# Kernel optimization log

Hardware: AMD Instinct MI355X
Metric: run time of the kernel (lower is better)

Reference implementation:

```python
import jax, jax.numpy as jnp
import numpy as np
from jax import lax

DT = 0.01  # fixed Euler-Maruyama step size

B, N, C, M, H, T = 1024, 64, 16, 16, 512, 128


def setup_inputs() -> dict:
    key = jax.random.key(0)
    ks = jax.random.split(key, 8)
    d_in = N + C  # concat(y, control)
    inp = {
        "y0": jax.random.normal(ks[0], (B, N), jnp.float32),
        "controls": jax.random.normal(ks[1], (T, C), jnp.float32),
        "noise": jax.random.normal(ks[2], (T - 1, B, M), jnp.float32),
        # mu MLP: d_in -> H -> N
        "W1_mu": jax.random.normal(ks[3], (d_in, H), jnp.float32) / np.sqrt(d_in),
        "b1_mu": jnp.zeros((H,), jnp.float32),
        "W2_mu": jax.random.normal(ks[4], (H, N), jnp.float32) / np.sqrt(H),
        "b2_mu": jnp.zeros((N,), jnp.float32),
        # sigma MLP: d_in -> H -> N*M
        "W1_sg": jax.random.normal(ks[5], (d_in, H), jnp.float32) / np.sqrt(d_in),
        "b1_sg": jnp.zeros((H,), jnp.float32),
        "W2_sg": jax.random.normal(ks[6], (H, N * M), jnp.float32) / np.sqrt(H),
        "b2_sg": jnp.zeros((N * M,), jnp.float32),
    }
    return inp


def _mlp(x, W1, b1, W2, b2):
    return jnp.maximum(x @ W1 + b1, 0.0) @ W2 + b2


def reference(y0, controls, noise, W1_mu, b1_mu, W2_mu, b2_mu,
              W1_sg, b1_sg, W2_sg, b2_sg):
    """Euler-Maruyama solve of dy = f(y,u) dt + g(y,u) dW.
    Returns trajectory [T, B, N] including y0 (as torchsde.sdeint does)."""
    b, n = y0.shape
    m = noise.shape[-1]
    sqrt_dt = jnp.sqrt(jnp.asarray(DT, y0.dtype))

    def step(y, inp):
        u, z = inp  # u: [C] control at t_k, z: [B, M] standard normal
        x = jnp.concatenate([y, jnp.broadcast_to(u[None, :], (b, u.shape[0]))], axis=1)
        drift = _mlp(x, W1_mu, b1_mu, W2_mu, b2_mu)              # [B, N]
        diff = _mlp(x, W1_sg, b1_sg, W2_sg, b2_sg).reshape(b, n, m)  # [B, N, M]
        dW = z * sqrt_dt
        y_next = y + drift * DT + jnp.einsum('bnm,bm->bn', diff, dW)
        return y_next, y_next

    _, ys = lax.scan(step, y0, (controls[:-1], noise))
    return jnp.concatenate([y0[None], ys], axis=0)  # [T, B, N]
```

## Files before the change

### kernel.cpp

```cpp
#include <hip/hip_runtime.h>


typedef _Float16 f16x8 __attribute__((ext_vector_type(8)));
typedef float    f32x4 __attribute__((ext_vector_type(4)));

#define MFMA(a,b,c) __builtin_amdgcn_mfma_f32_16x16x32_f16(a,b,c,0,0,0)

#define Bb 1024
#define Tt 128
#define NG 64
#define GB 8
#define Rr 16
#define NT 512

#define W2SG_OFF 0
#define W2SG_HALVES (64*16*2*512)
#define W2MU_OFF (W2SG_OFF + W2SG_HALVES)
#define W2MU_HALVES (4*16*2*512)
#define W1MU_OFF (W2MU_OFF + W2MU_HALVES)
#define W1_HALVES (32*3*2*512)
#define W1SG_OFF (W1MU_OFF + W1_HALVES)
#define WS_HALVES (W1SG_OFF + W1_HALVES)
#define ACC_BYTES_OFF ((size_t)WS_HALVES * 2)
#define ACC_FLOATS (3 * NG * 1024)
#define CNT_BYTES_OFF (ACC_BYTES_OFF + (size_t)ACC_FLOATS * 4)
#define CNT_STRIDE 16

__global__ __launch_bounds__(256) void pack_weights(
    const float* __restrict__ W1_mu, const float* __restrict__ W2_mu,
    const float* __restrict__ W1_sg, const float* __restrict__ W2_sg,
    _Float16* __restrict__ wsh)
{
    int gid = blockIdx.x * 256 + threadIdx.x;
    if (gid >= 81920) return;
    const float* src; int ncols, kvalid; size_t dst;
    int id, tile, ks, lane;
    if (gid < 65536) {
        id = gid; tile = id >> 10; id &= 1023; ks = id >> 6; lane = id & 63;
        src = W2_sg; ncols = 1024; kvalid = 512;
        dst = W2SG_OFF + (size_t)((tile*16 + ks)*2) * 512 + lane*8;
    } else if (gid < 69632) {
        id = gid - 65536; tile = id >> 10; id &= 1023; ks = id >> 6; lane = id & 63;
        src = W2_mu; ncols = 64; kvalid = 512;
        dst = W2MU_OFF + (size_t)((tile*16 + ks)*2) * 512 + lane*8;
    } else if (gid < 75776) {
        id = gid - 69632; tile = id / 192; id %= 192; ks = id >> 6; lane = id & 63;
        src = W1_mu; ncols = 512; kvalid = 80;
        dst = W1MU_OFF + (size_t)((tile*3 + ks)*2) * 512 + lane*8;
    } else {
        id = gid - 75776; tile = id / 192; id %= 192; ks = id >> 6; lane = id & 63;
        src = W1_sg; ncols = 512; kvalid = 80;
        dst = W1SG_OFF + (size_t)((tile*3 + ks)*2) * 512 + lane*8;
    }
    const int n  = tile*16 + (lane & 15);
    const int kb = ks*32 + ((lane >> 4) << 3);
    f16x8 hi8, lo8;
    #pragma unroll
    for (int jj = 0; jj < 8; ++jj) {
        int k = kb + jj;
        float wv = (k < kvalid) ? src[(size_t)k * ncols + n] : 0.f;
        _Float16 h = (_Float16)wv;
        hi8[jj] = h;
        lo8[jj] = (_Float16)(wv - (float)h);
    }
    *((f16x8*)(wsh + dst))       = hi8;
    *((f16x8*)(wsh + dst + 512)) = lo8;
}

__global__ __launch_bounds__(NT, 4) void nsde_splitk(
    const float* __restrict__ y0, const float* __restrict__ controls,
    const float* __restrict__ noise,
    const float* __restrict__ b1_mu, const float* __restrict__ b2_mu,
    const float* __restrict__ b1_sg, const float* __restrict__ b2_sg,
    const _Float16* __restrict__ wf,
    float* __restrict__ accbuf, unsigned int* __restrict__ cnt,
    float* __restrict__ out)
{
    __shared__ _Float16 s_xhi[Rr][104], s_xlo[Rr][104];
    __shared__ _Float16 s_hhi[2][Rr][72], s_hlo[2][Rr][72];
    __shared__ float s_y[Rr*64];
    __shared__ float s_dw[Rr][16];
    __shared__ float s_part[Rr*64];
    __shared__ float s_pmu[Rr*64];

    const int tid  = threadIdx.x;
    const int lane = tid & 63, w = tid >> 6;
    const int m15  = lane & 15, quad = lane >> 4;
    const int j    = blockIdx.x & 7;
    const int g    = blockIdx.x >> 3;
    const int r0   = g * Rr;

    const int l  = w >> 2;
    const int ct = w & 3;
    const int tg = j*4 + ct;
    const _Float16* w1base = wf + (l ? W1SG_OFF : W1MU_OFF);
    const float bias1 = (l ? b1_sg : b1_mu)[j*64 + ct*16 + m15];
    float b2v[8];
    #pragma unroll
    for (int t = 0; t < 8; ++t)
        b2v[t] = (j == 0) ? b2_sg[(w + t*8)*16 + m15] : 0.f;
    const float b2m = (w < 4 && j == 0) ? b2_mu[w*16 + m15] * 0.01f : 0.f;

    for (int e = tid; e < Rr*24; e += NT) {
        int r = e / 24, c = 80 + e % 24;
        s_xhi[r][c] = (_Float16)0.f; s_xlo[r][c] = (_Float16)0.f;
    }
    if (tid < 256) {
        int e0 = tid*4, r = e0 >> 6, n = e0 & 63;
        float4 yv = *(const float4*)&y0[(size_t)(r0 + r)*64 + n];
        float vv[4] = {yv.x, yv.y, yv.z, yv.w};
        #pragma unroll
        for (int q = 0; q < 4; ++q) {
            s_y[e0+q] = vv[q];
            _Float16 h = (_Float16)vv[q];
            s_xhi[r][n+q] = h; s_xlo[r][n+q] = (_Float16)(vv[q] - (float)h);
        }
        if ((tid >> 5) == j)
            *(float4*)&out[(size_t)(r0 + r)*64 + n] = yv;
        int rr2 = tid >> 4, cc2 = tid & 15;
        float u = controls[cc2];
        _Float16 h = (_Float16)u;
        s_xhi[rr2][64+cc2] = h; s_xlo[rr2][64+cc2] = (_Float16)(u - (float)h);
        s_dw[rr2][cc2] = noise[(size_t)(r0 + rr2)*16 + cc2] * 0.1f;
    }
    __syncthreads();

    for (int k = 0; k < Tt-1; ++k) {
        {
            f32x4 a0 = {0,0,0,0}, a1 = {0,0,0,0}, a2 = {0,0,0,0};
            #pragma unroll
            for (int ks = 0; ks < 3; ++ks) {
                const _Float16* bp = w1base + (size_t)((tg*3 + ks)*2)*512 + lane*8;
                f16x8 bh = *(const f16x8*)bp;
                f16x8 bl = *(const f16x8*)(bp + 512);
                f16x8 ah = *(const f16x8*)&s_xhi[m15][ks*32 + quad*8];
                f16x8 al = *(const f16x8*)&s_xlo[m15][ks*32 + quad*8];
                a0 = MFMA(ah, bh, a0);
                a1 = MFMA(ah, bl, a1);
                a2 = MFMA(al, bh, a2);
            }
            f32x4 s = a0 + a1 + a2;
            #pragma unroll
            for (int rg = 0; rg < 4; ++rg) {
                int row = quad*4 + rg;
                float v = fmaxf(s[rg] + bias1, 0.f);
                _Float16 h = (_Float16)v;
                s_hhi[l][row][ct*16 + m15] = h;
                s_hlo[l][row][ct*16 + m15] = (_Float16)(v - (float)h);
            }
        }
        __syncthreads();

        float dwv[4];
        #pragma unroll
        for (int rg = 0; rg < 4; ++rg)
            dwv[rg] = s_dw[quad*4 + rg][m15];

        if (w < 4) {
            f16x8 Mh0 = *(const f16x8*)&s_hhi[0][m15][quad*8];
            f16x8 Ml0 = *(const f16x8*)&s_hlo[0][m15][quad*8];
            f16x8 Mh1 = *(const f16x8*)&s_hhi[0][m15][32 + quad*8];
            f16x8 Ml1 = *(const f16x8*)&s_hlo[0][m15][32 + quad*8];
            const _Float16* bp = wf + W2MU_OFF + (size_t)((w*16 + 2*j)*2)*512 + lane*8;
            f16x8 bh0 = *(const f16x8*)(bp);
            f16x8 bl0 = *(const f16x8*)(bp + 512);
            f16x8 bh1 = *(const f16x8*)(bp + 1024);
            f16x8 bl1 = *(const f16x8*)(bp + 1536);
            f32x4 hh = {0,0,0,0}, hl = {0,0,0,0}, lh = {0,0,0,0};
            hh = MFMA(Mh0, bh0, hh); hl = MFMA(Mh0, bl0, hl); lh = MFMA(Ml0, bh0, lh);
            hh = MFMA(Mh1, bh1, hh); hl = MFMA(Mh1, bl1, hl); lh = MFMA(Ml1, bh1, lh);
            f32x4 s = hh + hl + lh;
            #pragma unroll
            for (int rg = 0; rg < 4; ++rg)
                s_pmu[(quad*4 + rg)*64 + w*16 + m15] = s[rg]*0.01f + b2m;
        }

        f16x8 Ah0 = *(const f16x8*)&s_hhi[1][m15][quad*8];
        f16x8 Al0 = *(const f16x8*)&s_hlo[1][m15][quad*8];
        f16x8 Ah1 = *(const f16x8*)&s_hhi[1][m15][32 + quad*8];
        f16x8 Al1 = *(const f16x8*)&s_hlo[1][m15][32 + quad*8];
        #pragma unroll 2
        for (int t = 0; t < 8; ++t) {
            const int nt = w + t*8;
            const _Float16* bp = wf + W2SG_OFF + (size_t)((nt*16 + 2*j)*2)*512 + lane*8;
            f16x8 bh0 = *(const f16x8*)(bp);
            f16x8 bl0 = *(const f16x8*)(bp + 512);
            f16x8 bh1 = *(const f16x8*)(bp + 1024);
            f16x8 bl1 = *(const f16x8*)(bp + 1536);
            f32x4 hh = {0,0,0,0}, hl = {0,0,0,0}, lh = {0,0,0,0};
            hh = MFMA(Ah0, bh0, hh); hl = MFMA(Ah0, bl0, hl); lh = MFMA(Al0, bh0, lh);
            hh = MFMA(Ah1, bh1, hh); hl = MFMA(Ah1, bl1, hl); lh = MFMA(Al1, bh1, lh);
            f32x4 s = hh + hl + lh;
            #pragma unroll
            for (int rg = 0; rg < 4; ++rg) {
                float v = (s[rg] + b2v[t]) * dwv[rg];
                v += __shfl_xor(v, 1); v += __shfl_xor(v, 2);
                v += __shfl_xor(v, 4); v += __shfl_xor(v, 8);
                if (m15 == 0) s_part[(quad*4 + rg)*64 + nt] = v;
            }
        }
        __syncthreads();

        const int slot = k % 3;
        float* ab = accbuf + ((size_t)slot*NG + g)*1024;
        const int e0 = tid*2;
        {
            float v0 = s_part[e0]   + s_pmu[e0];
            float v1 = s_part[e0+1] + s_pmu[e0+1];
            __hip_atomic_fetch_add(&ab[e0],   v0, __ATOMIC_RELAXED,
                                   __HIP_MEMORY_SCOPE_AGENT);
            __hip_atomic_fetch_add(&ab[e0+1], v1, __ATOMIC_RELAXED,
                                   __HIP_MEMORY_SCOPE_AGENT);
        }
        __syncthreads();
        if (tid == 0) {
            __hip_atomic_fetch_add(&cnt[g*CNT_STRIDE], 1u, __ATOMIC_RELEASE,
                                   __HIP_MEMORY_SCOPE_AGENT);
            while (__hip_atomic_load(&cnt[g*CNT_STRIDE], __ATOMIC_RELAXED,
                                     __HIP_MEMORY_SCOPE_AGENT) < (unsigned)GB*(k+1))
                __builtin_amdgcn_s_sleep(2);
        }
        __syncthreads();

        {
            const int r = e0 >> 6, n = e0 & 63;
            float sum0 = __hip_atomic_load(&ab[e0], __ATOMIC_RELAXED,
                                           __HIP_MEMORY_SCOPE_AGENT);
            float sum1 = __hip_atomic_load(&ab[e0+1], __ATOMIC_RELAXED,
                                           __HIP_MEMORY_SCOPE_AGENT);
            float ya = s_y[e0]   + sum0;
            float yb = s_y[e0+1] + sum1;
            s_y[e0] = ya; s_y[e0+1] = yb;
            _Float16 ha = (_Float16)ya, hb = (_Float16)yb;
            s_xhi[r][n] = ha;   s_xlo[r][n]   = (_Float16)(ya - (float)ha);
            s_xhi[r][n+1] = hb; s_xlo[r][n+1] = (_Float16)(yb - (float)hb);
            if ((tid >> 6) == j) {
                float2 o = {ya, yb};
                *(float2*)&out[((size_t)(k+1)*Bb + r0 + r)*64 + n] = o;
                if (k >= 1) {
                    float* zb = accbuf + ((size_t)((k-1)%3)*NG + g)*1024;
                    __hip_atomic_store(&zb[e0],   0.f, __ATOMIC_RELAXED,
                                       __HIP_MEMORY_SCOPE_AGENT);
                    __hip_atomic_store(&zb[e0+1], 0.f, __ATOMIC_RELAXED,
                                       __HIP_MEMORY_SCOPE_AGENT);
                }
            }
        }
        if (k < Tt-2 && tid < 256) {
            int r = tid >> 4, c = tid & 15;
            float u = controls[(size_t)(k+1)*16 + c];
            _Float16 h = (_Float16)u;
            s_xhi[r][64+c] = h; s_xlo[r][64+c] = (_Float16)(u - (float)h);
            s_dw[r][c] = noise[((size_t)(k+1)*Bb + r0 + r)*16 + c] * 0.1f;
        }
        __syncthreads();
    }
}

extern "C" void kernel_launch(void* const* d_in, const int* in_sizes, int n_in,
                              void* d_out, int out_size, void* d_ws, size_t ws_size,
                              hipStream_t stream) {
    const float* y0       = (const float*)d_in[0];
    const float* controls = (const float*)d_in[1];
    const float* noise    = (const float*)d_in[2];
    const float* W1_mu    = (const float*)d_in[3];
    const float* b1_mu    = (const float*)d_in[4];
    const float* W2_mu    = (const float*)d_in[5];
    const float* b2_mu    = (const float*)d_in[6];
    const float* W1_sg    = (const float*)d_in[7];
    const float* b1_sg    = (const float*)d_in[8];
    const float* W2_sg    = (const float*)d_in[9];
    const float* b2_sg    = (const float*)d_in[10];
    float* out = (float*)d_out;
    _Float16* wsh = (_Float16*)d_ws;
    float* accbuf = (float*)((char*)d_ws + ACC_BYTES_OFF);
    unsigned int* cnt = (unsigned int*)((char*)d_ws + CNT_BYTES_OFF);

    hipMemsetAsync((char*)d_ws + ACC_BYTES_OFF, 0,
                   (size_t)ACC_FLOATS*4 + (size_t)NG*CNT_STRIDE*4, stream);
    pack_weights<<<320, 256, 0, stream>>>(W1_mu, W2_mu, W1_sg, W2_sg, wsh);
    nsde_splitk<<<NG*GB, NT, 0, stream>>>(y0, controls, noise,
                                          b1_mu, b2_mu, b1_sg, b2_sg,
                                          (const _Float16*)wsh,
                                          accbuf, cnt, out);
}
```

Before: 2.297 ms.

## Keep weight fragments resident in registers and double rows per block

The per-step weight fragments (W1, W2_mu, W2_sg hi/lo) are loaded once into registers before the time loop instead of being reloaded from global memory every step. Each block now handles 32 rows instead of 16, so there are half as many blocks (256) and each runs two M-tiles per step. Next-step control and noise loads are issued before the barrier to overlap with compute. In exchange, register pressure rises sharply (launch bounds drop to 2 blocks per CU) and there are fewer groups, and therefore fewer blocks, spinning on the cross-block counter.

```diff
diff --git a/kernel.cpp b/kernel.cpp
--- a/kernel.cpp
+++ b/kernel.cpp
@@ -8,9 +8,9 @@
 
 #define Bb 1024
 #define Tt 128
-#define NG 64
+#define NG 32
 #define GB 8
-#define Rr 16
+#define Rr 32
 #define NT 512
 
 #define W2SG_OFF 0
@@ -22,7 +22,7 @@
 #define W1SG_OFF (W1MU_OFF + W1_HALVES)
 #define WS_HALVES (W1SG_OFF + W1_HALVES)
 #define ACC_BYTES_OFF ((size_t)WS_HALVES * 2)
-#define ACC_FLOATS (3 * NG * 1024)
+#define ACC_FLOATS (3 * NG * Rr * 64)
 #define CNT_BYTES_OFF (ACC_BYTES_OFF + (size_t)ACC_FLOATS * 4)
 #define CNT_STRIDE 16
 
@@ -67,7 +67,7 @@
     *((f16x8*)(wsh + dst + 512)) = lo8;
 }
 
-__global__ __launch_bounds__(NT, 4) void nsde_splitk(
+__global__ __launch_bounds__(NT, 2) void nsde_regw(
     const float* __restrict__ y0, const float* __restrict__ controls,
     const float* __restrict__ noise,
     const float* __restrict__ b1_mu, const float* __restrict__ b2_mu,
@@ -93,7 +93,6 @@
     const int l  = w >> 2;
     const int ct = w & 3;
     const int tg = j*4 + ct;
-    const _Float16* w1base = wf + (l ? W1SG_OFF : W1MU_OFF);
     const float bias1 = (l ? b1_sg : b1_mu)[j*64 + ct*16 + m15];
     float b2v[8];
     #pragma unroll
@@ -101,12 +100,43 @@
         b2v[t] = (j == 0) ? b2_sg[(w + t*8)*16 + m15] : 0.f;
     const float b2m = (w < 4 && j == 0) ? b2_mu[w*16 + m15] * 0.01f : 0.f;
 
+    f16x8 w1h[3], w1l[3];
+    {
+        const _Float16* w1base = wf + (l ? W1SG_OFF : W1MU_OFF);
+        #pragma unroll
+        for (int ks = 0; ks < 3; ++ks) {
+            const _Float16* bp = w1base + (size_t)((tg*3 + ks)*2)*512 + lane*8;
+            w1h[ks] = *(const f16x8*)bp;
+            w1l[ks] = *(const f16x8*)(bp + 512);
+        }
+    }
+    f16x8 wsg[8][4];
+    #pragma unroll
+    for (int t = 0; t < 8; ++t) {
+        const _Float16* bp = wf + W2SG_OFF
+            + (size_t)(((w + t*8)*16 + 2*j)*2)*512 + lane*8;
+        wsg[t][0] = *(const f16x8*)(bp);
+        wsg[t][1] = *(const f16x8*)(bp + 512);
+        wsg[t][2] = *(const f16x8*)(bp + 1024);
+        wsg[t][3] = *(const f16x8*)(bp + 1536);
+    }
+    f16x8 wmu[4];
+    {
+        const int wm = w & 3;
+        const _Float16* bp = wf + W2MU_OFF
+            + (size_t)((wm*16 + 2*j)*2)*512 + lane*8;
+        wmu[0] = *(const f16x8*)(bp);
+        wmu[1] = *(const f16x8*)(bp + 512);
+        wmu[2] = *(const f16x8*)(bp + 1024);
+        wmu[3] = *(const f16x8*)(bp + 1536);
+    }
+
     for (int e = tid; e < Rr*24; e += NT) {
         int r = e / 24, c = 80 + e % 24;
         s_xhi[r][c] = (_Float16)0.f; s_xlo[r][c] = (_Float16)0.f;
     }
-    if (tid < 256) {
-        int e0 = tid*4, r = e0 >> 6, n = e0 & 63;
+    {
+        const int e0 = tid*4, r = e0 >> 6, n = e0 & 63;
         float4 yv = *(const float4*)&y0[(size_t)(r0 + r)*64 + n];
         float vv[4] = {yv.x, yv.y, yv.z, yv.w};
         #pragma unroll
@@ -115,101 +145,101 @@
             _Float16 h = (_Float16)vv[q];
             s_xhi[r][n+q] = h; s_xlo[r][n+q] = (_Float16)(vv[q] - (float)h);
         }
-        if ((tid >> 5) == j)
+        if ((tid >> 6) == j)
             *(float4*)&out[(size_t)(r0 + r)*64 + n] = yv;
-        int rr2 = tid >> 4, cc2 = tid & 15;
-        float u = controls[cc2];
+        const int r2 = tid >> 4, c2 = tid & 15;
+        float u = controls[c2];
         _Float16 h = (_Float16)u;
-        s_xhi[rr2][64+cc2] = h; s_xlo[rr2][64+cc2] = (_Float16)(u - (float)h);
-        s_dw[rr2][cc2] = noise[(size_t)(r0 + rr2)*16 + cc2] * 0.1f;
+        s_xhi[r2][64+c2] = h; s_xlo[r2][64+c2] = (_Float16)(u - (float)h);
+        s_dw[r2][c2] = noise[(size_t)(r0 + r2)*16 + c2] * 0.1f;
     }
     __syncthreads();
 
     for (int k = 0; k < Tt-1; ++k) {
-        {
+        #pragma unroll
+        for (int mt = 0; mt < 2; ++mt) {
             f32x4 a0 = {0,0,0,0}, a1 = {0,0,0,0}, a2 = {0,0,0,0};
             #pragma unroll
             for (int ks = 0; ks < 3; ++ks) {
-                const _Float16* bp = w1base + (size_t)((tg*3 + ks)*2)*512 + lane*8;
-                f16x8 bh = *(const f16x8*)bp;
-                f16x8 bl = *(const f16x8*)(bp + 512);
-                f16x8 ah = *(const f16x8*)&s_xhi[m15][ks*32 + quad*8];
-                f16x8 al = *(const f16x8*)&s_xlo[m15][ks*32 + quad*8];
-                a0 = MFMA(ah, bh, a0);
-                a1 = MFMA(ah, bl, a1);
-                a2 = MFMA(al, bh, a2);
+                f16x8 ah = *(const f16x8*)&s_xhi[mt*16 + m15][ks*32 + quad*8];
+                f16x8 al = *(const f16x8*)&s_xlo[mt*16 + m15][ks*32 + quad*8];
+                a0 = MFMA(ah, w1h[ks], a0);
+                a1 = MFMA(ah, w1l[ks], a1);
+                a2 = MFMA(al, w1h[ks], a2);
             }
             f32x4 s = a0 + a1 + a2;
             #pragma unroll
             for (int rg = 0; rg < 4; ++rg) {
-                int row = quad*4 + rg;
+                int row = mt*16 + quad*4 + rg;
                 float v = fmaxf(s[rg] + bias1, 0.f);
                 _Float16 h = (_Float16)v;
                 s_hhi[l][row][ct*16 + m15] = h;
                 s_hlo[l][row][ct*16 + m15] = (_Float16)(v - (float)h);
             }
         }
-        __syncthreads();
-
-        float dwv[4];
-        #pragma unroll
-        for (int rg = 0; rg < 4; ++rg)
-            dwv[rg] = s_dw[quad*4 + rg][m15];
-
-        if (w < 4) {
-            f16x8 Mh0 = *(const f16x8*)&s_hhi[0][m15][quad*8];
-            f16x8 Ml0 = *(const f16x8*)&s_hlo[0][m15][quad*8];
-            f16x8 Mh1 = *(const f16x8*)&s_hhi[0][m15][32 + quad*8];
-            f16x8 Ml1 = *(const f16x8*)&s_hlo[0][m15][32 + quad*8];
-            const _Float16* bp = wf + W2MU_OFF + (size_t)((w*16 + 2*j)*2)*512 + lane*8;
-            f16x8 bh0 = *(const f16x8*)(bp);
-            f16x8 bl0 = *(const f16x8*)(bp + 512);
-            f16x8 bh1 = *(const f16x8*)(bp + 1024);
-            f16x8 bl1 = *(const f16x8*)(bp + 1536);
-            f32x4 hh = {0,0,0,0}, hl = {0,0,0,0}, lh = {0,0,0,0};
-            hh = MFMA(Mh0, bh0, hh); hl = MFMA(Mh0, bl0, hl); lh = MFMA(Ml0, bh0, lh);
-            hh = MFMA(Mh1, bh1, hh); hl = MFMA(Mh1, bl1, hl); lh = MFMA(Ml1, bh1, lh);
-            f32x4 s = hh + hl + lh;
+        float u_nx = 0.f, dw_nx = 0.f;
+        const int r2 = tid >> 4, c2 = tid & 15;
+        if (k < Tt-2) {
+            u_nx  = controls[(size_t)(k+1)*16 + c2];
+            dw_nx = noise[((size_t)(k+1)*Bb + r0 + r2)*16 + c2] * 0.1f;
+        }
+        __syncthreads();
+
+        #pragma unroll
+        for (int mt = 0; mt < 2; ++mt) {
+            const int rb = mt*16;
+            float dwv[4];
             #pragma unroll
             for (int rg = 0; rg < 4; ++rg)
-                s_pmu[(quad*4 + rg)*64 + w*16 + m15] = s[rg]*0.01f + b2m;
-        }
-
-        f16x8 Ah0 = *(const f16x8*)&s_hhi[1][m15][quad*8];
-        f16x8 Al0 = *(const f16x8*)&s_hlo[1][m15][quad*8];
-        f16x8 Ah1 = *(const f16x8*)&s_hhi[1][m15][32 + quad*8];
-        f16x8 Al1 = *(const f16x8*)&s_hlo[1][m15][32 + quad*8];
-        #pragma unroll 2
-        for (int t = 0; t < 8; ++t) {
-            const int nt = w + t*8;
-            const _Float16* bp = wf + W2SG_OFF + (size_t)((nt*16 + 2*j)*2)*512 + lane*8;
-            f16x8 bh0 = *(const f16x8*)(bp);
-            f16x8 bl0 = *(const f16x8*)(bp + 512);
-            f16x8 bh1 = *(const f16x8*)(bp + 1024);
-            f16x8 bl1 = *(const f16x8*)(bp + 1536);
-            f32x4 hh = {0,0,0,0}, hl = {0,0,0,0}, lh = {0,0,0,0};
-            hh = MFMA(Ah0, bh0, hh); hl = MFMA(Ah0, bl0, hl); lh = MFMA(Al0, bh0, lh);
-            hh = MFMA(Ah1, bh1, hh); hl = MFMA(Ah1, bl1, hl); lh = MFMA(Al1, bh1, lh);
-            f32x4 s = hh + hl + lh;
-            #pragma unroll
-            for (int rg = 0; rg < 4; ++rg) {
-                float v = (s[rg] + b2v[t]) * dwv[rg];
-                v += __shfl_xor(v, 1); v += __shfl_xor(v, 2);
-                v += __shfl_xor(v, 4); v += __shfl_xor(v, 8);
-                if (m15 == 0) s_part[(quad*4 + rg)*64 + nt] = v;
+                dwv[rg] = s_dw[rb + quad*4 + rg][m15];
+
+            if (w < 4) {
+                f16x8 Mh0 = *(const f16x8*)&s_hhi[0][rb + m15][quad*8];
+                f16x8 Ml0 = *(const f16x8*)&s_hlo[0][rb + m15][quad*8];
+                f16x8 Mh1 = *(const f16x8*)&s_hhi[0][rb + m15][32 + quad*8];
+                f16x8 Ml1 = *(const f16x8*)&s_hlo[0][rb + m15][32 + quad*8];
+                f32x4 hh = {0,0,0,0}, hl = {0,0,0,0}, lh = {0,0,0,0};
+                hh = MFMA(Mh0, wmu[0], hh); hl = MFMA(Mh0, wmu[1], hl);
+                lh = MFMA(Ml0, wmu[0], lh);
+                hh = MFMA(Mh1, wmu[2], hh); hl = MFMA(Mh1, wmu[3], hl);
+                lh = MFMA(Ml1, wmu[2], lh);
+                f32x4 s = hh + hl + lh;
+                #pragma unroll
+                for (int rg = 0; rg < 4; ++rg)
+                    s_pmu[(rb + quad*4 + rg)*64 + w*16 + m15] = s[rg]*0.01f + b2m;
+            }
+
+            f16x8 Ah0 = *(const f16x8*)&s_hhi[1][rb + m15][quad*8];
+            f16x8 Al0 = *(const f16x8*)&s_hlo[1][rb + m15][quad*8];
+            f16x8 Ah1 = *(const f16x8*)&s_hhi[1][rb + m15][32 + quad*8];
+            f16x8 Al1 = *(const f16x8*)&s_hlo[1][rb + m15][32 + quad*8];
+            #pragma unroll
+            for (int t = 0; t < 8; ++t) {
+                const int nt = w + t*8;
+                f32x4 hh = {0,0,0,0}, hl = {0,0,0,0}, lh = {0,0,0,0};
+                hh = MFMA(Ah0, wsg[t][0], hh); hl = MFMA(Ah0, wsg[t][1], hl);
+                lh = MFMA(Al0, wsg[t][0], lh);
+                hh = MFMA(Ah1, wsg[t][2], hh); hl = MFMA(Ah1, wsg[t][3], hl);
+                lh = MFMA(Al1, wsg[t][2], lh);
+                f32x4 s = hh + hl + lh;
+                #pragma unroll
+                for (int rg = 0; rg < 4; ++rg) {
+                    float v = (s[rg] + b2v[t]) * dwv[rg];
+                    v += __shfl_xor(v, 1); v += __shfl_xor(v, 2);
+                    v += __shfl_xor(v, 4); v += __shfl_xor(v, 8);
+                    if (m15 == 0) s_part[(rb + quad*4 + rg)*64 + nt] = v;
+                }
             }
         }
         __syncthreads();
 
         const int slot = k % 3;
-        float* ab = accbuf + ((size_t)slot*NG + g)*1024;
-        const int e0 = tid*2;
-        {
-            float v0 = s_part[e0]   + s_pmu[e0];
-            float v1 = s_part[e0+1] + s_pmu[e0+1];
-            __hip_atomic_fetch_add(&ab[e0],   v0, __ATOMIC_RELAXED,
-                                   __HIP_MEMORY_SCOPE_AGENT);
-            __hip_atomic_fetch_add(&ab[e0+1], v1, __ATOMIC_RELAXED,
+        float* ab = accbuf + ((size_t)slot*NG + g)*(Rr*64);
+        const int e0 = tid*4;
+        #pragma unroll
+        for (int q = 0; q < 4; ++q) {
+            float v = s_part[e0+q] + s_pmu[e0+q];
+            __hip_atomic_fetch_add(&ab[e0+q], v, __ATOMIC_RELAXED,
                                    __HIP_MEMORY_SCOPE_AGENT);
         }
         __syncthreads();
@@ -224,34 +254,33 @@
 
         {
             const int r = e0 >> 6, n = e0 & 63;
-            float sum0 = __hip_atomic_load(&ab[e0], __ATOMIC_RELAXED,
+            float yn[4];
+            #pragma unroll
+            for (int q = 0; q < 4; ++q) {
+                float sum = __hip_atomic_load(&ab[e0+q], __ATOMIC_RELAXED,
+                                              __HIP_MEMORY_SCOPE_AGENT);
+                yn[q] = s_y[e0+q] + sum;
+                s_y[e0+q] = yn[q];
+                _Float16 h = (_Float16)yn[q];
+                s_xhi[r][n+q] = h;
+                s_xlo[r][n+q] = (_Float16)(yn[q] - (float)h);
+            }
+            if ((tid >> 6) == j) {
+                float4 o = {yn[0], yn[1], yn[2], yn[3]};
+                *(float4*)&out[((size_t)(k+1)*Bb + r0 + r)*64 + n] = o;
+                if (k >= 1) {
+                    float* zb = accbuf + ((size_t)((k-1)%3)*NG + g)*(Rr*64);
+                    #pragma unroll
+                    for (int q = 0; q < 4; ++q)
+                        __hip_atomic_store(&zb[e0+q], 0.f, __ATOMIC_RELAXED,
                                            __HIP_MEMORY_SCOPE_AGENT);
-            float sum1 = __hip_atomic_load(&ab[e0+1], __ATOMIC_RELAXED,
-                                           __HIP_MEMORY_SCOPE_AGENT);
-            float ya = s_y[e0]   + sum0;
-            float yb = s_y[e0+1] + sum1;
-            s_y[e0] = ya; s_y[e0+1] = yb;
-            _Float16 ha = (_Float16)ya, hb = (_Float16)yb;
-            s_xhi[r][n] = ha;   s_xlo[r][n]   = (_Float16)(ya - (float)ha);
-            s_xhi[r][n+1] = hb; s_xlo[r][n+1] = (_Float16)(yb - (float)hb);
-            if ((tid >> 6) == j) {
-                float2 o = {ya, yb};
-                *(float2*)&out[((size_t)(k+1)*Bb + r0 + r)*64 + n] = o;
-                if (k >= 1) {
-                    float* zb = accbuf + ((size_t)((k-1)%3)*NG + g)*1024;
-                    __hip_atomic_store(&zb[e0],   0.f, __ATOMIC_RELAXED,
-                                       __HIP_MEMORY_SCOPE_AGENT);
-                    __hip_atomic_store(&zb[e0+1], 0.f, __ATOMIC_RELAXED,
-                                       __HIP_MEMORY_SCOPE_AGENT);
                 }
             }
         }
-        if (k < Tt-2 && tid < 256) {
-            int r = tid >> 4, c = tid & 15;
-            float u = controls[(size_t)(k+1)*16 + c];
-            _Float16 h = (_Float16)u;
-            s_xhi[r][64+c] = h; s_xlo[r][64+c] = (_Float16)(u - (float)h);
-            s_dw[r][c] = noise[((size_t)(k+1)*Bb + r0 + r)*16 + c] * 0.1f;
+        if (k < Tt-2) {
+            _Float16 h = (_Float16)u_nx;
+            s_xhi[r2][64+c2] = h; s_xlo[r2][64+c2] = (_Float16)(u_nx - (float)h);
+            s_dw[r2][c2] = dw_nx;
         }
         __syncthreads();
     }
@@ -279,8 +308,8 @@
     hipMemsetAsync((char*)d_ws + ACC_BYTES_OFF, 0,
                    (size_t)ACC_FLOATS*4 + (size_t)NG*CNT_STRIDE*4, stream);
     pack_weights<<<320, 256, 0, stream>>>(W1_mu, W2_mu, W1_sg, W2_sg, wsh);
-    nsde_splitk<<<NG*GB, NT, 0, stream>>>(y0, controls, noise,
-                                          b1_mu, b2_mu, b1_sg, b2_sg,
-                                          (const _Float16*)wsh,
-                                          accbuf, cnt, out);
+    nsde_regw<<<NG*GB, NT, 0, stream>>>(y0, controls, noise,
+                                        b1_mu, b2_mu, b1_sg, b2_sg,
+                                        (const _Float16*)wsh,
+                                        accbuf, cnt, out);
 }
```

After: 2.755 ms. +19.9%, slower.

## Replace atomic split-K reduction with per-block partial stores and reader-side sum

Applied to the files above, without the earlier changes.

Each block in a group now writes its partial update into its own slot with plain stores instead of atomically adding into a shared accumulator. After the group barrier, every block reads all eight partials and sums them in a fixed order. This removes atomic contention and the per-step zeroing of old slots, and shrinks the memset to just the counters. It also hoists the next step's control and noise global loads before an earlier barrier to hide their latency. The cost is eight times more reads per step and a larger workspace buffer. Dropping from three slots to two relies on the monotonic counter barrier to keep a fast block from overwriting a slot another block is still reading.

```diff
diff --git a/kernel.cpp b/kernel.cpp
--- a/kernel.cpp
+++ b/kernel.cpp
@@ -22,7 +22,7 @@
 #define W1SG_OFF (W1MU_OFF + W1_HALVES)
 #define WS_HALVES (W1SG_OFF + W1_HALVES)
 #define ACC_BYTES_OFF ((size_t)WS_HALVES * 2)
-#define ACC_FLOATS (3 * NG * 1024)
+#define ACC_FLOATS (2 * NG * GB * 1024)
 #define CNT_BYTES_OFF (ACC_BYTES_OFF + (size_t)ACC_FLOATS * 4)
 #define CNT_STRIDE 16
 
@@ -67,7 +67,7 @@
     *((f16x8*)(wsh + dst + 512)) = lo8;
 }
 
-__global__ __launch_bounds__(NT, 4) void nsde_splitk(
+__global__ __launch_bounds__(NT, 4) void nsde_store(
     const float* __restrict__ y0, const float* __restrict__ controls,
     const float* __restrict__ noise,
     const float* __restrict__ b1_mu, const float* __restrict__ b2_mu,
@@ -148,6 +148,12 @@
                 s_hhi[l][row][ct*16 + m15] = h;
                 s_hlo[l][row][ct*16 + m15] = (_Float16)(v - (float)h);
             }
+        }
+        float u_nx = 0.f, dw_nx = 0.f;
+        const int r2 = tid >> 4, c2 = tid & 15;
+        if (k < Tt-2 && tid < 256) {
+            u_nx  = controls[(size_t)(k+1)*16 + c2];
+            dw_nx = noise[((size_t)(k+1)*Bb + r0 + r2)*16 + c2] * 0.1f;
         }
         __syncthreads();
 
@@ -201,16 +207,16 @@
         }
         __syncthreads();
 
-        const int slot = k % 3;
-        float* ab = accbuf + ((size_t)slot*NG + g)*1024;
+        const int slot = k & 1;
+        float* ab = accbuf + (((size_t)slot*NG + g)*GB + j)*1024;
         const int e0 = tid*2;
         {
             float v0 = s_part[e0]   + s_pmu[e0];
             float v1 = s_part[e0+1] + s_pmu[e0+1];
-            __hip_atomic_fetch_add(&ab[e0],   v0, __ATOMIC_RELAXED,
-                                   __HIP_MEMORY_SCOPE_AGENT);
-            __hip_atomic_fetch_add(&ab[e0+1], v1, __ATOMIC_RELAXED,
-                                   __HIP_MEMORY_SCOPE_AGENT);
+            __hip_atomic_store(&ab[e0],   v0, __ATOMIC_RELAXED,
+                               __HIP_MEMORY_SCOPE_AGENT);
+            __hip_atomic_store(&ab[e0+1], v1, __ATOMIC_RELAXED,
+                               __HIP_MEMORY_SCOPE_AGENT);
         }
         __syncthreads();
         if (tid == 0) {
@@ -224,10 +230,17 @@
 
         {
             const int r = e0 >> 6, n = e0 & 63;
-            float sum0 = __hip_atomic_load(&ab[e0], __ATOMIC_RELAXED,
-                                           __HIP_MEMORY_SCOPE_AGENT);
-            float sum1 = __hip_atomic_load(&ab[e0+1], __ATOMIC_RELAXED,
-                                           __HIP_MEMORY_SCOPE_AGENT);
+            const float* rb = accbuf + (((size_t)slot*NG + g)*GB)*1024;
+            float a0[GB], a1[GB];
+            #pragma unroll
+            for (int b = 0; b < GB; ++b) {
+                a0[b] = __hip_atomic_load(&rb[(size_t)b*1024 + e0],
+                                          __ATOMIC_RELAXED, __HIP_MEMORY_SCOPE_AGENT);
+                a1[b] = __hip_atomic_load(&rb[(size_t)b*1024 + e0 + 1],
+                                          __ATOMIC_RELAXED, __HIP_MEMORY_SCOPE_AGENT);
+            }
+            float sum0 = ((a0[0]+a0[1])+(a0[2]+a0[3]))+((a0[4]+a0[5])+(a0[6]+a0[7]));
+            float sum1 = ((a1[0]+a1[1])+(a1[2]+a1[3]))+((a1[4]+a1[5])+(a1[6]+a1[7]));
             float ya = s_y[e0]   + sum0;
             float yb = s_y[e0+1] + sum1;
             s_y[e0] = ya; s_y[e0+1] = yb;
@@ -237,21 +250,12 @@
             if ((tid >> 6) == j) {
                 float2 o = {ya, yb};
                 *(float2*)&out[((size_t)(k+1)*Bb + r0 + r)*64 + n] = o;
-                if (k >= 1) {
-                    float* zb = accbuf + ((size_t)((k-1)%3)*NG + g)*1024;
-                    __hip_atomic_store(&zb[e0],   0.f, __ATOMIC_RELAXED,
-                                       __HIP_MEMORY_SCOPE_AGENT);
-                    __hip_atomic_store(&zb[e0+1], 0.f, __ATOMIC_RELAXED,
-                                       __HIP_MEMORY_SCOPE_AGENT);
-                }
             }
         }
         if (k < Tt-2 && tid < 256) {
-            int r = tid >> 4, c = tid & 15;
-            float u = controls[(size_t)(k+1)*16 + c];
-            _Float16 h = (_Float16)u;
-            s_xhi[r][64+c] = h; s_xlo[r][64+c] = (_Float16)(u - (float)h);
-            s_dw[r][c] = noise[((size_t)(k+1)*Bb + r0 + r)*16 + c] * 0.1f;
+            _Float16 h = (_Float16)u_nx;
+            s_xhi[r2][64+c2] = h; s_xlo[r2][64+c2] = (_Float16)(u_nx - (float)h);
+            s_dw[r2][c2] = dw_nx;
         }
         __syncthreads();
     }
@@ -276,11 +280,11 @@
     float* accbuf = (float*)((char*)d_ws + ACC_BYTES_OFF);
     unsigned int* cnt = (unsigned int*)((char*)d_ws + CNT_BYTES_OFF);
 
-    hipMemsetAsync((char*)d_ws + ACC_BYTES_OFF, 0,
-                   (size_t)ACC_FLOATS*4 + (size_t)NG*CNT_STRIDE*4, stream);
+    hipMemsetAsync((char*)d_ws + CNT_BYTES_OFF, 0,
+                   (size_t)NG*CNT_STRIDE*4, stream);
     pack_weights<<<320, 256, 0, stream>>>(W1_mu, W2_mu, W1_sg, W2_sg, wsh);
-    nsde_splitk<<<NG*GB, NT, 0, stream>>>(y0, controls, noise,
-                                          b1_mu, b2_mu, b1_sg, b2_sg,
-                                          (const _Float16*)wsh,
-                                          accbuf, cnt, out);
+    nsde_store<<<NG*GB, NT, 0, stream>>>(y0, controls, noise,
+                                         b1_mu, b2_mu, b1_sg, b2_sg,
+                                         (const _Float16*)wsh,
+                                         accbuf, cnt, out);
 }
```

After: 2.821 ms. 22.8% more time.

## Split hidden dimension across 16 blocks per batch group instead of 8

Applied to the files above, without the earlier changes.

Doubles the number of cooperating blocks per 16-row batch group, so each block owns 32 hidden units instead of 64. This halves per-block MFMA work and weight loads in both layers, and raises occupancy bounds to 8 blocks per CU. Next-step control and noise loads are also issued earlier, before a barrier, to hide their latency. In exchange, twice as many blocks contend on the global atomic accumulation and counter spin-wait each step, and only half the waves do first-layer work.

```diff
diff --git a/kernel.cpp b/kernel.cpp
--- a/kernel.cpp
+++ b/kernel.cpp
@@ -9,7 +9,7 @@
 #define Bb 1024
 #define Tt 128
 #define NG 64
-#define GB 8
+#define GB 16
 #define Rr 16
 #define NT 512
 
@@ -67,7 +67,7 @@
     *((f16x8*)(wsh + dst + 512)) = lo8;
 }
 
-__global__ __launch_bounds__(NT, 4) void nsde_splitk(
+__global__ __launch_bounds__(NT, 8) void nsde_gb16(
     const float* __restrict__ y0, const float* __restrict__ controls,
     const float* __restrict__ noise,
     const float* __restrict__ b1_mu, const float* __restrict__ b2_mu,
@@ -77,7 +77,7 @@
     float* __restrict__ out)
 {
     __shared__ _Float16 s_xhi[Rr][104], s_xlo[Rr][104];
-    __shared__ _Float16 s_hhi[2][Rr][72], s_hlo[2][Rr][72];
+    __shared__ _Float16 s_hhi[2][Rr][40], s_hlo[2][Rr][40];
     __shared__ float s_y[Rr*64];
     __shared__ float s_dw[Rr][16];
     __shared__ float s_part[Rr*64];
@@ -86,15 +86,15 @@
     const int tid  = threadIdx.x;
     const int lane = tid & 63, w = tid >> 6;
     const int m15  = lane & 15, quad = lane >> 4;
-    const int j    = blockIdx.x & 7;
-    const int g    = blockIdx.x >> 3;
+    const int j    = blockIdx.x & 15;
+    const int g    = blockIdx.x >> 4;
     const int r0   = g * Rr;
 
-    const int l  = w >> 2;
-    const int ct = w & 3;
-    const int tg = j*4 + ct;
+    const int l  = w >> 1;
+    const int ct = w & 1;
+    const int tg = j*2 + ct;
     const _Float16* w1base = wf + (l ? W1SG_OFF : W1MU_OFF);
-    const float bias1 = (l ? b1_sg : b1_mu)[j*64 + ct*16 + m15];
+    const float bias1 = (w < 4) ? (l ? b1_sg : b1_mu)[j*32 + ct*16 + m15] : 0.f;
     float b2v[8];
     #pragma unroll
     for (int t = 0; t < 8; ++t)
@@ -115,7 +115,7 @@
             _Float16 h = (_Float16)vv[q];
             s_xhi[r][n+q] = h; s_xlo[r][n+q] = (_Float16)(vv[q] - (float)h);
         }
-        if ((tid >> 5) == j)
+        if ((tid >> 4) == j)
             *(float4*)&out[(size_t)(r0 + r)*64 + n] = yv;
         int rr2 = tid >> 4, cc2 = tid & 15;
         float u = controls[cc2];
@@ -126,7 +126,7 @@
     __syncthreads();
 
     for (int k = 0; k < Tt-1; ++k) {
-        {
+        if (w < 4) {
             f32x4 a0 = {0,0,0,0}, a1 = {0,0,0,0}, a2 = {0,0,0,0};
             #pragma unroll
             for (int ks = 0; ks < 3; ++ks) {
@@ -149,6 +149,12 @@
                 s_hlo[l][row][ct*16 + m15] = (_Float16)(v - (float)h);
             }
         }
+        float u_nx = 0.f, dw_nx = 0.f;
+        const int r2 = tid >> 4, c2 = tid & 15;
+        if (k < Tt-2 && tid < 256) {
+            u_nx  = controls[(size_t)(k+1)*16 + c2];
+            dw_nx = noise[((size_t)(k+1)*Bb + r0 + r2)*16 + c2] * 0.1f;
+        }
         __syncthreads();
 
         float dwv[4];
@@ -159,16 +165,11 @@
         if (w < 4) {
             f16x8 Mh0 = *(const f16x8*)&s_hhi[0][m15][quad*8];
             f16x8 Ml0 = *(const f16x8*)&s_hlo[0][m15][quad*8];
-            f16x8 Mh1 = *(const f16x8*)&s_hhi[0][m15][32 + quad*8];
-            f16x8 Ml1 = *(const f16x8*)&s_hlo[0][m15][32 + quad*8];
-            const _Float16* bp = wf + W2MU_OFF + (size_t)((w*16 + 2*j)*2)*512 + lane*8;
+            const _Float16* bp = wf + W2MU_OFF + (size_t)((w*16 + j)*2)*512 + lane*8;
             f16x8 bh0 = *(const f16x8*)(bp);
             f16x8 bl0 = *(const f16x8*)(bp + 512);
-            f16x8 bh1 = *(const f16x8*)(bp + 1024);
-            f16x8 bl1 = *(const f16x8*)(bp + 1536);
             f32x4 hh = {0,0,0,0}, hl = {0,0,0,0}, lh = {0,0,0,0};
             hh = MFMA(Mh0, bh0, hh); hl = MFMA(Mh0, bl0, hl); lh = MFMA(Ml0, bh0, lh);
-            hh = MFMA(Mh1, bh1, hh); hl = MFMA(Mh1, bl1, hl); lh = MFMA(Ml1, bh1, lh);
             f32x4 s = hh + hl + lh;
             #pragma unroll
             for (int rg = 0; rg < 4; ++rg)
@@ -177,19 +178,14 @@
 
         f16x8 Ah0 = *(const f16x8*)&s_hhi[1][m15][quad*8];
         f16x8 Al0 = *(const f16x8*)&s_hlo[1][m15][quad*8];
-        f16x8 Ah1 = *(const f16x8*)&s_hhi[1][m15][32 + quad*8];
-        f16x8 Al1 = *(const f16x8*)&s_hlo[1][m15][32 + quad*8];
         #pragma unroll 2
         for (int t = 0; t < 8; ++t) {
             const int nt = w + t*8;
-            const _Float16* bp = wf + W2SG_OFF + (size_t)((nt*16 + 2*j)*2)*512 + lane*8;
+            const _Float16* bp = wf + W2SG_OFF + (size_t)((nt*16 + j)*2)*512 + lane*8;
             f16x8 bh0 = *(const f16x8*)(bp);
             f16x8 bl0 = *(const f16x8*)(bp + 512);
-            f16x8 bh1 = *(const f16x8*)(bp + 1024);
-            f16x8 bl1 = *(const f16x8*)(bp + 1536);
             f32x4 hh = {0,0,0,0}, hl = {0,0,0,0}, lh = {0,0,0,0};
             hh = MFMA(Ah0, bh0, hh); hl = MFMA(Ah0, bl0, hl); lh = MFMA(Al0, bh0, lh);
-            hh = MFMA(Ah1, bh1, hh); hl = MFMA(Ah1, bl1, hl); lh = MFMA(Al1, bh1, lh);
             f32x4 s = hh + hl + lh;
             #pragma unroll
             for (int rg = 0; rg < 4; ++rg) {
@@ -234,7 +230,7 @@
             _Float16 ha = (_Float16)ya, hb = (_Float16)yb;
             s_xhi[r][n] = ha;   s_xlo[r][n]   = (_Float16)(ya - (float)ha);
             s_xhi[r][n+1] = hb; s_xlo[r][n+1] = (_Float16)(yb - (float)hb);
-            if ((tid >> 6) == j) {
+            if ((tid >> 5) == j) {
                 float2 o = {ya, yb};
                 *(float2*)&out[((size_t)(k+1)*Bb + r0 + r)*64 + n] = o;
                 if (k >= 1) {
@@ -247,11 +243,9 @@
             }
         }
         if (k < Tt-2 && tid < 256) {
-            int r = tid >> 4, c = tid & 15;
-            float u = controls[(size_t)(k+1)*16 + c];
-            _Float16 h = (_Float16)u;
-            s_xhi[r][64+c] = h; s_xlo[r][64+c] = (_Float16)(u - (float)h);
-            s_dw[r][c] = noise[((size_t)(k+1)*Bb + r0 + r)*16 + c] * 0.1f;
+            _Float16 h = (_Float16)u_nx;
+            s_xhi[r2][64+c2] = h; s_xlo[r2][64+c2] = (_Float16)(u_nx - (float)h);
+            s_dw[r2][c2] = dw_nx;
         }
         __syncthreads();
     }
@@ -279,8 +273,8 @@
     hipMemsetAsync((char*)d_ws + ACC_BYTES_OFF, 0,
                    (size_t)ACC_FLOATS*4 + (size_t)NG*CNT_STRIDE*4, stream);
     pack_weights<<<320, 256, 0, stream>>>(W1_mu, W2_mu, W1_sg, W2_sg, wsh);
-    nsde_splitk<<<NG*GB, NT, 0, stream>>>(y0, controls, noise,
-                                          b1_mu, b2_mu, b1_sg, b2_sg,
-                                          (const _Float16*)wsh,
-                                          accbuf, cnt, out);
+    nsde_gb16<<<NG*GB, NT, 0, stream>>>(y0, controls, noise,
+                                        b1_mu, b2_mu, b1_sg, b2_sg,
+                                        (const _Float16*)wsh,
+                                        accbuf, cnt, out);
 }
```

Measured after the change: 4.421 ms. 92.4% more time.
